# Optimization experiments

Measured on AMD Instinct MI355X. Metric: run time of the kernel, lower is better.

Reference implementation:

```python
import jax, jax.numpy as jnp
import numpy as np

N = 2_000_000  # total nodes across batch
F = 16         # eigenvector coefficient dim
B = 8          # number of graphs in batch (2^B sign combos)

def setup_inputs() -> dict:
    key = jax.random.key(0)
    k1, k2, k3 = jax.random.split(key, 3)
    inp = jax.random.normal(k1, (N, F), dtype=jnp.float32)
    tgt = jax.random.normal(k2, (N, F), dtype=jnp.float32)
    batch = jnp.sort(jax.random.randint(k3, (N,), 0, B, dtype=jnp.int32))
    return {"input": inp, "target": tgt, "batch": batch, "batch_size": B}

def reference(input, target, batch, batch_size):
    # loss(s) = sum((s_{batch} * x - t)^2) = sum(x^2) + sum(t^2) - 2 * sum_g s_g * dot_g
    # where dot_g = sum_{i in graph g} <x_i, t_i>.  Min over s in {+1,-1}^B is the
    # exact value produced by the original 2^B brute-force loop (reduction='sum').
    per_node = jnp.sum(input * target, axis=-1)                      # [N]
    dots = jax.ops.segment_sum(per_node, batch, num_segments=batch_size)  # [B]
    base = jnp.sum(input * input) + jnp.sum(target * target)         # scalar
    # enumerate all 2^B sign combinations (tiny, graph-level)
    idx = jnp.arange(2 ** batch_size)
    bits = (idx[:, None] >> jnp.arange(batch_size)[None, :]) & 1     # [2^B, B]
    signs = (1 - 2 * bits).astype(dots.dtype)                        # {+1,-1}
    losses = base - 2.0 * (signs @ dots)                             # [2^B]
    return jnp.min(losses)
```

## Files before the change

kernel.cpp:

```cpp
#include <hip/hip_runtime.h>

#define BLOCK 256
#define GRID  2048
#define NGRAPH 8


__global__ __launch_bounds__(BLOCK) void reduce_kernel(
    const float4* __restrict__ x4,
    const float4* __restrict__ t4,
    const int*    __restrict__ batch,
    float* __restrict__ g_acc,
    long long M )
{
    __shared__ float s_dots[NGRAPH];
    __shared__ float s_base;
    const int tid = threadIdx.x;
    if (tid < NGRAPH) s_dots[tid] = 0.0f;
    if (tid == 0)     s_base = 0.0f;
    __syncthreads();

    const long long stride = (long long)gridDim.x * (long long)blockDim.x;
    const long long start  = (long long)blockIdx.x * blockDim.x + tid;
    const long long M_pad = ((M + stride - 1) / stride) * stride;

    float base = 0.0f;

    for (long long e = start; e < M_pad; e += stride) {
        const bool valid = (e < M);
        float4 a = make_float4(0.f, 0.f, 0.f, 0.f);
        float4 c = make_float4(0.f, 0.f, 0.f, 0.f);
        int b = 0;
        if (valid) {
            a = x4[e];
            c = t4[e];
            b = batch[e >> 2];
        }
        base += a.x*a.x + a.y*a.y + a.z*a.z + a.w*a.w
              + c.x*c.x + c.y*c.y + c.z*c.z + c.w*c.w;
        float d = a.x*c.x + a.y*c.y + a.z*c.z + a.w*c.w;

        const int b0 = __builtin_amdgcn_readfirstlane(b);
        if (__all(b == b0)) {
            for (int off = 32; off > 0; off >>= 1)
                d += __shfl_xor(d, off, 64);
            if ((tid & 63) == 0)
                atomicAdd(&s_dots[b0], d);
        } else {
            atomicAdd(&s_dots[b], d);
        }
    }

    for (int off = 32; off > 0; off >>= 1)
        base += __shfl_xor(base, off, 64);
    if ((tid & 63) == 0)
        atomicAdd(&s_base, base);
    __syncthreads();

    if (tid < NGRAPH) atomicAdd(&g_acc[tid], s_dots[tid]);
    if (tid == 0)     atomicAdd(&g_acc[NGRAPH], s_base);
}

__global__ void finalize_kernel(const float* __restrict__ g_acc,
                                float* __restrict__ out)
{
    if (threadIdx.x == 0) {
        float s = 0.0f;
        #pragma unroll
        for (int i = 0; i < NGRAPH; ++i) s += fabsf(g_acc[i]);
        out[0] = g_acc[NGRAPH] - 2.0f * s;
    }
}

extern "C" void kernel_launch(void* const* d_in, const int* in_sizes, int n_in,
                              void* d_out, int out_size, void* d_ws, size_t ws_size,
                              hipStream_t stream) {
    const float* inp   = (const float*)d_in[0];
    const float* tgt   = (const float*)d_in[1];
    const int*   batch = (const int*)d_in[2];

    const long long Nrows = (long long)in_sizes[0] / 16;
    const long long M     = Nrows * 4;

    float* g_acc = (float*)d_ws;
    hipMemsetAsync(g_acc, 0, (NGRAPH + 1) * sizeof(float), stream);

    reduce_kernel<<<GRID, BLOCK, 0, stream>>>(
        (const float4*)inp, (const float4*)tgt, batch, g_acc, M);

    finalize_kernel<<<1, 64, 0, stream>>>(g_acc, (float*)d_out);
}
```

Before: 304.0 us.

## Use contiguous block chunks, per-thread segment accumulation, and fuse finalize via last-block

Each block now handles a contiguous chunk of the data rather than grid-striding. Each thread keeps a running per-graph dot sum and flushes it to shared memory with an atomic only when the graph id changes, which replaces the per-iteration wave ballot, shuffle reduction and atomic. The separate finalize kernel is removed: a global counter picks the last block to finish, and that block computes the output, saving one kernel launch. Per-block chunking may reduce coalescing locality across the grid, and the last-block pattern relies on threadfence ordering.

```diff
diff --git a/kernel.cpp b/kernel.cpp
--- a/kernel.cpp
+++ b/kernel.cpp
@@ -10,45 +10,45 @@
     const float4* __restrict__ t4,
     const int*    __restrict__ batch,
     float* __restrict__ g_acc,
+    int*   __restrict__ d_count,
+    float* __restrict__ out,
     long long M )
 {
     __shared__ float s_dots[NGRAPH];
     __shared__ float s_base;
+    __shared__ int   s_last;
     const int tid = threadIdx.x;
     if (tid < NGRAPH) s_dots[tid] = 0.0f;
     if (tid == 0)     s_base = 0.0f;
     __syncthreads();
 
-    const long long stride = (long long)gridDim.x * (long long)blockDim.x;
-    const long long start  = (long long)blockIdx.x * blockDim.x + tid;
-    const long long M_pad = ((M + stride - 1) / stride) * stride;
+    const long long chunk =
+        ((M + (long long)GRID * BLOCK - 1) / ((long long)GRID * BLOCK)) * BLOCK;
+    long long s0 = (long long)blockIdx.x * chunk;
+    long long s1 = s0 + chunk;
+    if (s1 > M) s1 = M;
 
-    float base = 0.0f;
+    float base  = 0.0f;
+    float d_acc = 0.0f;
+    int   b_cur = 0;
+    if (s0 + tid < M) b_cur = batch[(s0 + tid) >> 2];
 
-    for (long long e = start; e < M_pad; e += stride) {
-        const bool valid = (e < M);
-        float4 a = make_float4(0.f, 0.f, 0.f, 0.f);
-        float4 c = make_float4(0.f, 0.f, 0.f, 0.f);
-        int b = 0;
-        if (valid) {
-            a = x4[e];
-            c = t4[e];
-            b = batch[e >> 2];
-        }
+    #pragma unroll 4
+    for (long long e = s0 + tid; e < s1; e += BLOCK) {
+        float4 a = x4[e];
+        float4 c = t4[e];
+        int b = batch[e >> 2];
         base += a.x*a.x + a.y*a.y + a.z*a.z + a.w*a.w
               + c.x*c.x + c.y*c.y + c.z*c.z + c.w*c.w;
         float d = a.x*c.x + a.y*c.y + a.z*c.z + a.w*c.w;
-
-        const int b0 = __builtin_amdgcn_readfirstlane(b);
-        if (__all(b == b0)) {
-            for (int off = 32; off > 0; off >>= 1)
-                d += __shfl_xor(d, off, 64);
-            if ((tid & 63) == 0)
-                atomicAdd(&s_dots[b0], d);
-        } else {
-            atomicAdd(&s_dots[b], d);
+        if (b != b_cur) {
+            atomicAdd(&s_dots[b_cur], d_acc);
+            d_acc = 0.0f;
+            b_cur = b;
         }
+        d_acc += d;
     }
+    atomicAdd(&s_dots[b_cur], d_acc);
 
     for (int off = 32; off > 0; off >>= 1)
         base += __shfl_xor(base, off, 64);
@@ -58,16 +58,25 @@
 
     if (tid < NGRAPH) atomicAdd(&g_acc[tid], s_dots[tid]);
     if (tid == 0)     atomicAdd(&g_acc[NGRAPH], s_base);
-}
 
-__global__ void finalize_kernel(const float* __restrict__ g_acc,
-                                float* __restrict__ out)
-{
-    if (threadIdx.x == 0) {
+    if (tid == 0) {
+        __threadfence();
+        int prev = atomicAdd(d_count, 1);
+        s_last = (prev == GRID - 1) ? 1 : 0;
+    }
+    __syncthreads();
+    if (tid == 0 && s_last) {
+        __threadfence();
         float s = 0.0f;
         #pragma unroll
-        for (int i = 0; i < NGRAPH; ++i) s += fabsf(g_acc[i]);
-        out[0] = g_acc[NGRAPH] - 2.0f * s;
+        for (int i = 0; i < NGRAPH; ++i) {
+            float v = __hip_atomic_load(&g_acc[i], __ATOMIC_RELAXED,
+                                        __HIP_MEMORY_SCOPE_AGENT);
+            s += fabsf(v);
+        }
+        float bs = __hip_atomic_load(&g_acc[NGRAPH], __ATOMIC_RELAXED,
+                                     __HIP_MEMORY_SCOPE_AGENT);
+        out[0] = bs - 2.0f * s;
     }
 }
 
@@ -81,11 +90,11 @@
     const long long Nrows = (long long)in_sizes[0] / 16;
     const long long M     = Nrows * 4;
 
-    float* g_acc = (float*)d_ws;
-    hipMemsetAsync(g_acc, 0, (NGRAPH + 1) * sizeof(float), stream);
+    float* g_acc   = (float*)d_ws;
+    int*   d_count = (int*)((float*)d_ws + NGRAPH + 1);
+    hipMemsetAsync(d_ws, 0, (NGRAPH + 1) * sizeof(float) + sizeof(int), stream);
 
     reduce_kernel<<<GRID, BLOCK, 0, stream>>>(
-        (const float4*)inp, (const float4*)tgt, batch, g_acc, M);
-
-    finalize_kernel<<<1, 64, 0, stream>>>(g_acc, (float*)d_out);
+        (const float4*)inp, (const float4*)tgt, batch, g_acc, d_count,
+        (float*)d_out, M);
 }
```

Result: slower. 372.9 us (+22.7%).
